# Optimization experiments

Measured on AMD Instinct MI355X. Metric: run time of the kernel, lower is better.

Reference implementation:

```python
import jax, jax.numpy as jnp
import numpy as np
from jax import lax

WIN_SIZE = 11
SIGMA = 1.5
K1, K2 = 0.01, 0.03
DATA_RANGE = 1.0


def _gauss_1d(size=WIN_SIZE, sigma=SIGMA):
    coords = jnp.arange(size, dtype=jnp.float32) - size // 2
    g = jnp.exp(-(coords ** 2) / (2.0 * sigma ** 2))
    return g / jnp.sum(g)


def _blur(x, win):
    # x: (1, C, H, W); separable depthwise gaussian, VALID padding (pytorch_msssim)
    C = x.shape[1]
    dn = ('NCHW', 'OIHW', 'NCHW')
    kw = jnp.tile(win.reshape(1, 1, 1, -1), (C, 1, 1, 1))  # (C,1,1,K)
    kh = jnp.tile(win.reshape(1, 1, -1, 1), (C, 1, 1, 1))  # (C,1,K,1)
    x = lax.conv_general_dilated(x, kw, (1, 1), 'VALID',
                                 dimension_numbers=dn, feature_group_count=C)
    x = lax.conv_general_dilated(x, kh, (1, 1), 'VALID',
                                 dimension_numbers=dn, feature_group_count=C)
    return x


def _ssim_loss(pred, targ, height, width):
    x = pred.reshape(1, 3, height, width)
    y = targ.reshape(1, 3, height, width)
    win = _gauss_1d()
    C1 = (K1 * DATA_RANGE) ** 2
    C2 = (K2 * DATA_RANGE) ** 2

    mu1 = _blur(x, win)
    mu2 = _blur(y, win)
    mu1_sq = mu1 * mu1
    mu2_sq = mu2 * mu2
    mu1_mu2 = mu1 * mu2
    sigma1_sq = _blur(x * x, win) - mu1_sq
    sigma2_sq = _blur(y * y, win) - mu2_sq
    sigma12 = _blur(x * y, win) - mu1_mu2

    cs_map = (2.0 * sigma12 + C2) / (sigma1_sq + sigma2_sq + C2)
    ssim_map = ((2.0 * mu1_mu2 + C1) / (mu1_sq + mu2_sq + C1)) * cs_map
    return 1.0 - jnp.mean(ssim_map)


def setup_inputs() -> dict:
    key = jax.random.key(0)
    k1, k2 = jax.random.split(key)
    H, W = 2048, 2048
    return {
        'predicted_img': jax.random.uniform(k1, (1, 3, H, W), dtype=jnp.float32),
        'target_img': jax.random.uniform(k2, (1, 3, H, W), dtype=jnp.float32),
        'height': H,
        'width': W,
    }


def reference(predicted_img, target_img, height, width):
    return _ssim_loss(predicted_img, target_img, height, width)
```

## Files before the change

kernel.cpp:

```cpp
#include <hip/hip_runtime.h>
#include <math.h>

typedef float f32x2 __attribute__((ext_vector_type(2)));
typedef float f32x4 __attribute__((ext_vector_type(4)));

#define HH    2048
#define WW    2048
#define NCH   3
#define NOUT  2038
#define OWID  64
#define OHGT  16
#define IHGT  26
#define SWP   76
#define HAW   66
#define HCW   68
#define NTX   32
#define NTY   128
#define NBLOCKS (NTX*NTY*NCH)
#define NOUT_TOTAL 12460332.0f

__device__ __forceinline__ float ssim_term(float mu1, float mu2,
                                           float b11, float b22, float b12) {
    const float c1v = 1e-4f, c2v = 9e-4f;
    float mu1sq = mu1 * mu1;
    float mu2sq = mu2 * mu2;
    float mu12  = mu1 * mu2;
    float s11 = b11 - mu1sq;
    float s22 = b22 - mu2sq;
    float s12 = b12 - mu12;
    float csn = 2.f * s12 + c2v;
    float csd = s11 + s22 + c2v;
    float ln  = 2.f * mu12 + c1v;
    float ld  = mu1sq + mu2sq + c1v;
    return (csn * ln) * __builtin_amdgcn_rcpf(csd * ld);
}

__global__ __launch_bounds__(256, 2)
void ssim_main(const float* __restrict__ x, const float* __restrict__ y,
               float* __restrict__ partials) {
    __shared__ f32x2 sxy[IHGT][SWP];
    __shared__ f32x2 hbA[IHGT][HAW];
    __shared__ f32x2 hbB[IHGT][HAW];
    __shared__ float hbC[IHGT][HCW];
    __shared__ float wsum[4];

    const int tid = threadIdx.x;
    const int gx0 = blockIdx.x * OWID;
    const int gy0 = blockIdx.y * OHGT;
    const float* xb = x + (size_t)blockIdx.z * HH * WW;
    const float* yb = y + (size_t)blockIdx.z * HH * WW;

    float w[11];
    {
        float s = 0.f;
        #pragma unroll
        for (int i = 0; i < 11; ++i) {
            float d = (float)(i - 5);
            w[i] = expf(-d * d / 4.5f);
            s += w[i];
        }
        float inv = 1.f / s;
        #pragma unroll
        for (int i = 0; i < 11; ++i) w[i] *= inv;
    }

    for (int u = tid; u < IHGT * 19; u += 256) {
        int r  = u / 19;
        int c0 = (u - r * 19) * 4;
        int gy = gy0 + r; if (gy > HH - 1) gy = HH - 1;
        const float* xr = xb + (size_t)gy * WW;
        const float* yr = yb + (size_t)gy * WW;
        int gxc = gx0 + c0;
        float4 xf, yf;
        if (gxc + 4 <= WW) {
            xf = *(const float4*)(xr + gxc);
            yf = *(const float4*)(yr + gxc);
        } else {
            int g0 = gxc     < WW ? gxc     : WW - 1;
            int g1 = gxc + 1 < WW ? gxc + 1 : WW - 1;
            int g2 = gxc + 2 < WW ? gxc + 2 : WW - 1;
            int g3 = gxc + 3 < WW ? gxc + 3 : WW - 1;
            xf = make_float4(xr[g0], xr[g1], xr[g2], xr[g3]);
            yf = make_float4(yr[g0], yr[g1], yr[g2], yr[g3]);
        }
        *(f32x4*)&sxy[r][c0]     = (f32x4){xf.x, yf.x, xf.y, yf.y};
        *(f32x4*)&sxy[r][c0 + 2] = (f32x4){xf.z, yf.z, xf.w, yf.w};
    }
    __syncthreads();

    for (int u = tid; u < IHGT * 16; u += 256) {
        int r  = u >> 4;
        int c0 = (u & 15) * 4;
        f32x2 p[16];
        #pragma unroll
        for (int t = 0; t < 8; ++t) {
            f32x4 raw = *(const f32x4*)&sxy[r][c0 + 2 * t];
            p[2 * t]     = (f32x2){raw.x, raw.y};
            p[2 * t + 1] = (f32x2){raw.z, raw.w};
        }
        f32x2 q[14]; float pr[14];
        #pragma unroll
        for (int t = 0; t < 14; ++t) {
            q[t]  = p[t] * p[t];
            pr[t] = p[t].x * p[t].y;
        }
        f32x2 hA[4] = {}, hB[4] = {};
        float hC[4] = {};
        #pragma unroll
        for (int k = 0; k < 11; ++k) {
            f32x2 wk2 = (f32x2){w[k], w[k]};
            #pragma unroll
            for (int j = 0; j < 4; ++j) {
                hA[j] = __builtin_elementwise_fma(wk2, p[j + k], hA[j]);
                hB[j] = __builtin_elementwise_fma(wk2, q[j + k], hB[j]);
                hC[j] = fmaf(w[k], pr[j + k], hC[j]);
            }
        }
        *(f32x4*)&hbA[r][c0]     = (f32x4){hA[0].x, hA[0].y, hA[1].x, hA[1].y};
        *(f32x4*)&hbA[r][c0 + 2] = (f32x4){hA[2].x, hA[2].y, hA[3].x, hA[3].y};
        *(f32x4*)&hbB[r][c0]     = (f32x4){hB[0].x, hB[0].y, hB[1].x, hB[1].y};
        *(f32x4*)&hbB[r][c0 + 2] = (f32x4){hB[2].x, hB[2].y, hB[3].x, hB[3].y};
        *(float4*)&hbC[r][c0]    = make_float4(hC[0], hC[1], hC[2], hC[3]);
    }
    __syncthreads();

    float partial = 0.f;
    {
        const int col = tid & 63;
        const int r0  = (tid >> 6) * 4;
        f32x2 vA[14], vB[14]; float vC[14];
        #pragma unroll
        for (int j = 0; j < 14; ++j) {
            vA[j] = hbA[r0 + j][col];
            vB[j] = hbB[r0 + j][col];
            vC[j] = hbC[r0 + j][col];
        }
        const int ocol = gx0 + col;
        #pragma unroll
        for (int i = 0; i < 4; ++i) {
            f32x2 aA = {0.f, 0.f}, aB = {0.f, 0.f};
            float aC = 0.f;
            #pragma unroll
            for (int k = 0; k < 11; ++k) {
                f32x2 wk2 = (f32x2){w[k], w[k]};
                aA = __builtin_elementwise_fma(wk2, vA[i + k], aA);
                aB = __builtin_elementwise_fma(wk2, vB[i + k], aB);
                aC = fmaf(w[k], vC[i + k], aC);
            }
            int orow = gy0 + r0 + i;
            if (orow < NOUT && ocol < NOUT)
                partial += ssim_term(aA.x, aA.y, aB.x, aB.y, aC);
        }
    }

    #pragma unroll
    for (int off = 32; off > 0; off >>= 1)
        partial += __shfl_down(partial, off, 64);
    if ((tid & 63) == 0) wsum[tid >> 6] = partial;
    __syncthreads();
    if (tid == 0) {
        int bid = (blockIdx.z * gridDim.y + blockIdx.y) * gridDim.x + blockIdx.x;
        partials[bid] = wsum[0] + wsum[1] + wsum[2] + wsum[3];
    }
}

__global__ __launch_bounds__(256)
void ssim_finalize(const float* __restrict__ partials, float* __restrict__ out) {
    __shared__ float ws[4];
    float s = 0.f;
    for (int i = threadIdx.x; i < NBLOCKS / 4; i += 256) {
        float4 v = ((const float4*)partials)[i];
        s += (v.x + v.y) + (v.z + v.w);
    }
    #pragma unroll
    for (int off = 32; off > 0; off >>= 1)
        s += __shfl_down(s, off, 64);
    if ((threadIdx.x & 63) == 0) ws[threadIdx.x >> 6] = s;
    __syncthreads();
    if (threadIdx.x == 0)
        out[0] = 1.f - (ws[0] + ws[1] + ws[2] + ws[3]) / NOUT_TOTAL;
}

extern "C" void kernel_launch(void* const* d_in, const int* in_sizes, int n_in,
                              void* d_out, int out_size, void* d_ws, size_t ws_size,
                              hipStream_t stream) {
    const float* x = (const float*)d_in[0];
    const float* y = (const float*)d_in[1];
    float* out = (float*)d_out;
    float* partials = (float*)d_ws;

    dim3 grid(NTX, NTY, NCH);
    ssim_main<<<grid, dim3(256), 0, stream>>>(x, y, partials);
    ssim_finalize<<<1, 256, 0, stream>>>(partials, out);
}
```

Before: 185.2 us.

## Shrink tile height to 11 rows and interleave blurred A/B in one LDS buffer

```diff
diff --git a/kernel.cpp b/kernel.cpp
--- a/kernel.cpp
+++ b/kernel.cpp
@@ -9,13 +9,13 @@
 #define NCH   3
 #define NOUT  2038
 #define OWID  64
-#define OHGT  16
-#define IHGT  26
+#define OHGT  11
+#define IHGT  21
 #define SWP   76
-#define HAW   66
-#define HCW   68
+#define HABW  64
+#define HCW   64
 #define NTX   32
-#define NTY   128
+#define NTY   186
 #define NBLOCKS (NTX*NTY*NCH)
 #define NOUT_TOTAL 12460332.0f
 
@@ -39,8 +39,7 @@
 void ssim_main(const float* __restrict__ x, const float* __restrict__ y,
                float* __restrict__ partials) {
     __shared__ f32x2 sxy[IHGT][SWP];
-    __shared__ f32x2 hbA[IHGT][HAW];
-    __shared__ f32x2 hbB[IHGT][HAW];
+    __shared__ f32x4 hbAB[IHGT][HABW];
     __shared__ float hbC[IHGT][HCW];
     __shared__ float wsum[4];
 
@@ -116,40 +115,44 @@
                 hC[j] = fmaf(w[k], pr[j + k], hC[j]);
             }
         }
-        *(f32x4*)&hbA[r][c0]     = (f32x4){hA[0].x, hA[0].y, hA[1].x, hA[1].y};
-        *(f32x4*)&hbA[r][c0 + 2] = (f32x4){hA[2].x, hA[2].y, hA[3].x, hA[3].y};
-        *(f32x4*)&hbB[r][c0]     = (f32x4){hB[0].x, hB[0].y, hB[1].x, hB[1].y};
-        *(f32x4*)&hbB[r][c0 + 2] = (f32x4){hB[2].x, hB[2].y, hB[3].x, hB[3].y};
-        *(float4*)&hbC[r][c0]    = make_float4(hC[0], hC[1], hC[2], hC[3]);
+        #pragma unroll
+        for (int j = 0; j < 4; ++j)
+            hbAB[r][c0 + j] = (f32x4){hA[j].x, hA[j].y, hB[j].x, hB[j].y};
+        *(float4*)&hbC[r][c0] = make_float4(hC[0], hC[1], hC[2], hC[3]);
     }
     __syncthreads();
 
     float partial = 0.f;
     {
         const int col = tid & 63;
-        const int r0  = (tid >> 6) * 4;
-        f32x2 vA[14], vB[14]; float vC[14];
+        const int rg  = tid >> 6;
+        const int r0  = rg * 3;
+        f32x4 vAB[13]; float vC[13];
         #pragma unroll
-        for (int j = 0; j < 14; ++j) {
-            vA[j] = hbA[r0 + j][col];
-            vB[j] = hbB[r0 + j][col];
-            vC[j] = hbC[r0 + j][col];
+        for (int j = 0; j < 13; ++j) {
+            int rr = r0 + j;
+            if (rr < IHGT) {
+                vAB[j] = hbAB[rr][col];
+                vC[j]  = hbC[rr][col];
+            } else {
+                vAB[j] = (f32x4){0.f, 0.f, 0.f, 0.f};
+                vC[j]  = 0.f;
+            }
         }
         const int ocol = gx0 + col;
         #pragma unroll
-        for (int i = 0; i < 4; ++i) {
-            f32x2 aA = {0.f, 0.f}, aB = {0.f, 0.f};
+        for (int i = 0; i < 3; ++i) {
+            f32x4 aAB = {0.f, 0.f, 0.f, 0.f};
             float aC = 0.f;
             #pragma unroll
             for (int k = 0; k < 11; ++k) {
-                f32x2 wk2 = (f32x2){w[k], w[k]};
-                aA = __builtin_elementwise_fma(wk2, vA[i + k], aA);
-                aB = __builtin_elementwise_fma(wk2, vB[i + k], aB);
-                aC = fmaf(w[k], vC[i + k], aC);
+                f32x4 wk4 = (f32x4){w[k], w[k], w[k], w[k]};
+                aAB = __builtin_elementwise_fma(wk4, vAB[i + k], aAB);
+                aC  = fmaf(w[k], vC[i + k], aC);
             }
             int orow = gy0 + r0 + i;
-            if (orow < NOUT && ocol < NOUT)
-                partial += ssim_term(aA.x, aA.y, aB.x, aB.y, aC);
+            if ((rg < 3 || i < 2) && orow < NOUT && ocol < NOUT)
+                partial += ssim_term(aAB.x, aAB.y, aAB.z, aAB.w, aC);
         }
     }
 
```

New measurement: 194.3 us. 1.05x slower.

## Stream tall output tiles with rolling ring buffer of horizontal blur rows

Applied to the files above, without the earlier changes.

```diff
diff --git a/kernel.cpp b/kernel.cpp
--- a/kernel.cpp
+++ b/kernel.cpp
@@ -9,13 +9,14 @@
 #define NCH   3
 #define NOUT  2038
 #define OWID  64
-#define OHGT  16
-#define IHGT  26
+#define OH    128
+#define CROWS 16
+#define BUF   32
 #define SWP   76
 #define HAW   66
 #define HCW   68
 #define NTX   32
-#define NTY   128
+#define NTY   16
 #define NBLOCKS (NTX*NTY*NCH)
 #define NOUT_TOTAL 12460332.0f
 
@@ -38,15 +39,15 @@
 __global__ __launch_bounds__(256, 2)
 void ssim_main(const float* __restrict__ x, const float* __restrict__ y,
                float* __restrict__ partials) {
-    __shared__ f32x2 sxy[IHGT][SWP];
-    __shared__ f32x2 hbA[IHGT][HAW];
-    __shared__ f32x2 hbB[IHGT][HAW];
-    __shared__ float hbC[IHGT][HCW];
+    __shared__ f32x2 sxy[CROWS][SWP];
+    __shared__ f32x2 hbA[BUF][HAW];
+    __shared__ f32x2 hbB[BUF][HAW];
+    __shared__ float hbC[BUF][HCW];
     __shared__ float wsum[4];
 
     const int tid = threadIdx.x;
     const int gx0 = blockIdx.x * OWID;
-    const int gy0 = blockIdx.y * OHGT;
+    const int gy0 = blockIdx.y * OH;
     const float* xb = x + (size_t)blockIdx.z * HH * WW;
     const float* yb = y + (size_t)blockIdx.z * HH * WW;
 
@@ -64,37 +65,39 @@
         for (int i = 0; i < 11; ++i) w[i] *= inv;
     }
 
-    for (int u = tid; u < IHGT * 19; u += 256) {
-        int r  = u / 19;
-        int c0 = (u - r * 19) * 4;
-        int gy = gy0 + r; if (gy > HH - 1) gy = HH - 1;
-        const float* xr = xb + (size_t)gy * WW;
-        const float* yr = yb + (size_t)gy * WW;
-        int gxc = gx0 + c0;
-        float4 xf, yf;
-        if (gxc + 4 <= WW) {
-            xf = *(const float4*)(xr + gxc);
-            yf = *(const float4*)(yr + gxc);
-        } else {
-            int g0 = gxc     < WW ? gxc     : WW - 1;
-            int g1 = gxc + 1 < WW ? gxc + 1 : WW - 1;
-            int g2 = gxc + 2 < WW ? gxc + 2 : WW - 1;
-            int g3 = gxc + 3 < WW ? gxc + 3 : WW - 1;
-            xf = make_float4(xr[g0], xr[g1], xr[g2], xr[g3]);
-            yf = make_float4(yr[g0], yr[g1], yr[g2], yr[g3]);
-        }
-        *(f32x4*)&sxy[r][c0]     = (f32x4){xf.x, yf.x, xf.y, yf.y};
-        *(f32x4*)&sxy[r][c0 + 2] = (f32x4){xf.z, yf.z, xf.w, yf.w};
-    }
-    __syncthreads();
-
-    for (int u = tid; u < IHGT * 16; u += 256) {
-        int r  = u >> 4;
-        int c0 = (u & 15) * 4;
+    auto loadA = [&](int base) {
+        for (int u = tid; u < CROWS * 19; u += 256) {
+            int lr = u / 19;
+            int c0 = (u - lr * 19) * 4;
+            int gy = gy0 + base + lr; if (gy > HH - 1) gy = HH - 1;
+            const float* xr = xb + (size_t)gy * WW;
+            const float* yr = yb + (size_t)gy * WW;
+            int gxc = gx0 + c0;
+            float4 xf, yf;
+            if (gxc + 4 <= WW) {
+                xf = *(const float4*)(xr + gxc);
+                yf = *(const float4*)(yr + gxc);
+            } else {
+                int g0 = gxc     < WW ? gxc     : WW - 1;
+                int g1 = gxc + 1 < WW ? gxc + 1 : WW - 1;
+                int g2 = gxc + 2 < WW ? gxc + 2 : WW - 1;
+                int g3 = gxc + 3 < WW ? gxc + 3 : WW - 1;
+                xf = make_float4(xr[g0], xr[g1], xr[g2], xr[g3]);
+                yf = make_float4(yr[g0], yr[g1], yr[g2], yr[g3]);
+            }
+            *(f32x4*)&sxy[lr][c0]     = (f32x4){xf.x, yf.x, xf.y, yf.y};
+            *(f32x4*)&sxy[lr][c0 + 2] = (f32x4){xf.z, yf.z, xf.w, yf.w};
+        }
+    };
+
+    auto blurB = [&](int base) {
+        int lr = tid >> 4;
+        int c0 = (tid & 15) * 4;
+        int slot = (base + lr) & (BUF - 1);
         f32x2 p[16];
         #pragma unroll
         for (int t = 0; t < 8; ++t) {
-            f32x4 raw = *(const f32x4*)&sxy[r][c0 + 2 * t];
+            f32x4 raw = *(const f32x4*)&sxy[lr][c0 + 2 * t];
             p[2 * t]     = (f32x2){raw.x, raw.y};
             p[2 * t + 1] = (f32x2){raw.z, raw.w};
         }
@@ -116,40 +119,52 @@
                 hC[j] = fmaf(w[k], pr[j + k], hC[j]);
             }
         }
-        *(f32x4*)&hbA[r][c0]     = (f32x4){hA[0].x, hA[0].y, hA[1].x, hA[1].y};
-        *(f32x4*)&hbA[r][c0 + 2] = (f32x4){hA[2].x, hA[2].y, hA[3].x, hA[3].y};
-        *(f32x4*)&hbB[r][c0]     = (f32x4){hB[0].x, hB[0].y, hB[1].x, hB[1].y};
-        *(f32x4*)&hbB[r][c0 + 2] = (f32x4){hB[2].x, hB[2].y, hB[3].x, hB[3].y};
-        *(float4*)&hbC[r][c0]    = make_float4(hC[0], hC[1], hC[2], hC[3]);
-    }
-    __syncthreads();
+        *(f32x4*)&hbA[slot][c0]     = (f32x4){hA[0].x, hA[0].y, hA[1].x, hA[1].y};
+        *(f32x4*)&hbA[slot][c0 + 2] = (f32x4){hA[2].x, hA[2].y, hA[3].x, hA[3].y};
+        *(f32x4*)&hbB[slot][c0]     = (f32x4){hB[0].x, hB[0].y, hB[1].x, hB[1].y};
+        *(f32x4*)&hbB[slot][c0 + 2] = (f32x4){hB[2].x, hB[2].y, hB[3].x, hB[3].y};
+        *(float4*)&hbC[slot][c0]    = make_float4(hC[0], hC[1], hC[2], hC[3]);
+    };
 
     float partial = 0.f;
-    {
-        const int col = tid & 63;
-        const int r0  = (tid >> 6) * 4;
-        f32x2 vA[14], vB[14]; float vC[14];
-        #pragma unroll
-        for (int j = 0; j < 14; ++j) {
-            vA[j] = hbA[r0 + j][col];
-            vB[j] = hbB[r0 + j][col];
-            vC[j] = hbC[r0 + j][col];
-        }
-        const int ocol = gx0 + col;
-        #pragma unroll
-        for (int i = 0; i < 4; ++i) {
-            f32x2 aA = {0.f, 0.f}, aB = {0.f, 0.f};
-            float aC = 0.f;
+
+    loadA(0);  __syncthreads(); blurB(0);  __syncthreads();
+    loadA(16); __syncthreads(); blurB(16); __syncthreads();
+
+    for (int m = 0; m < 8; ++m) {
+        const int o0 = m * CROWS;
+        {
+            const int col = tid & 63;
+            const int r0  = o0 + (tid >> 6) * 4;
+            f32x2 vA[14], vB[14]; float vC[14];
             #pragma unroll
-            for (int k = 0; k < 11; ++k) {
-                f32x2 wk2 = (f32x2){w[k], w[k]};
-                aA = __builtin_elementwise_fma(wk2, vA[i + k], aA);
-                aB = __builtin_elementwise_fma(wk2, vB[i + k], aB);
-                aC = fmaf(w[k], vC[i + k], aC);
-            }
-            int orow = gy0 + r0 + i;
-            if (orow < NOUT && ocol < NOUT)
-                partial += ssim_term(aA.x, aA.y, aB.x, aB.y, aC);
+            for (int j = 0; j < 14; ++j) {
+                int slot = (r0 + j) & (BUF - 1);
+                vA[j] = hbA[slot][col];
+                vB[j] = hbB[slot][col];
+                vC[j] = hbC[slot][col];
+            }
+            const int ocol = gx0 + col;
+            #pragma unroll
+            for (int i = 0; i < 4; ++i) {
+                f32x2 aA = {0.f, 0.f}, aB = {0.f, 0.f};
+                float aC = 0.f;
+                #pragma unroll
+                for (int k = 0; k < 11; ++k) {
+                    f32x2 wk2 = (f32x2){w[k], w[k]};
+                    aA = __builtin_elementwise_fma(wk2, vA[i + k], aA);
+                    aB = __builtin_elementwise_fma(wk2, vB[i + k], aB);
+                    aC = fmaf(w[k], vC[i + k], aC);
+                }
+                int orow = gy0 + r0 + i;
+                if (orow < NOUT && ocol < NOUT)
+                    partial += ssim_term(aA.x, aA.y, aB.x, aB.y, aC);
+            }
+        }
+        __syncthreads();
+        if (m < 7) {
+            loadA(32 + o0); __syncthreads();
+            blurB(32 + o0); __syncthreads();
         }
     }
 
```

Result: faster. 180.3 us (-2.7%).
